# Optimization experiments

Hardware: AMD Instinct MI355X
Metric: run time of the kernel (lower is better)

## Reference

```python
import jax, jax.numpy as jnp
import numpy as np

HIDDEN = 256   # HIDDEN_NUM
INPUT = 4      # fixed input_size
B, T = 128, 512


def _lstm_dir(xs, wi, wh, bi, bh):
    """Single-direction LSTM scan. xs: [T,B,D]; wi: [4H,D]; wh: [4H,H]; bi,bh: [4H].
    PyTorch gate order: i, f, g, o. Returns hidden states [T,B,H]."""
    Tn, Bn, _ = xs.shape
    Hn = wh.shape[1]
    # precompute input contribution for all timesteps (tiny D -> one big GEMM)
    gx = jnp.einsum('tbd,gd->tbg', xs, wi) + bi + bh  # [T,B,4H]

    def step(carry, g):
        h, c = carry
        g = g + h @ wh.T
        i, f, gg, o = jnp.split(g, 4, axis=-1)
        c = jax.nn.sigmoid(f) * c + jax.nn.sigmoid(i) * jnp.tanh(gg)
        h = jax.nn.sigmoid(o) * jnp.tanh(c)
        return (h, c), h

    init = (jnp.zeros((Bn, Hn), xs.dtype), jnp.zeros((Bn, Hn), xs.dtype))
    _, hs = jax.lax.scan(step, init, gx)
    return hs


def _lstm_bidir(xs, w_ih, w_hh, b_ih, b_hh):
    """xs: [T,B,D]; weights stacked over direction: w_ih [2,4H,D] etc. -> [T,B,2H]."""
    fwd = _lstm_dir(xs, w_ih[0], w_hh[0], b_ih[0], b_hh[0])
    bwd = _lstm_dir(xs[::-1], w_ih[1], w_hh[1], b_ih[1], b_hh[1])[::-1]
    return jnp.concatenate([fwd, bwd], axis=-1)


def setup_inputs() -> dict:
    key = jax.random.key(0)
    ks = jax.random.split(key, 12)
    k = 1.0 / np.sqrt(HIDDEN)
    u = lambda kk, shape: jax.random.uniform(kk, shape, jnp.float32, -k, k)
    H4 = 4 * HIDDEN
    return {
        'x': jax.random.normal(ks[0], (B, T, INPUT), jnp.float32),
        # layer 0 (input size 4), stacked [fwd, bwd]
        'w_ih0': u(ks[1], (2, H4, INPUT)),
        'w_hh0': u(ks[2], (2, H4, HIDDEN)),
        'b_ih0': u(ks[3], (2, H4)),
        'b_hh0': u(ks[4], (2, H4)),
        # layer 1 (input size 2H from bidirectional layer 0)
        'w_ih1': u(ks[5], (2, H4, 2 * HIDDEN)),
        'w_hh1': u(ks[6], (2, H4, HIDDEN)),
        'b_ih1': u(ks[7], (2, H4)),
        'b_hh1': u(ks[8], (2, H4)),
        # final linear: HIDDEN*2 -> 2
        'fc_w': u(ks[9], (2, 2 * HIDDEN)),
        'fc_b': u(ks[10], (2,)),
    }


def reference(x, w_ih0, w_hh0, b_ih0, b_hh0, w_ih1, w_hh1, b_ih1, b_hh1, fc_w, fc_b):
    xs = jnp.transpose(x, (1, 0, 2))                 # [T,B,4] (seq-major like torch)
    h0 = _lstm_bidir(xs, w_ih0, w_hh0, b_ih0, b_hh0)  # [T,B,2H]
    h1 = _lstm_bidir(h0, w_ih1, w_hh1, b_ih1, b_hh1)  # [T,B,2H]
    pooled = jnp.mean(h1, axis=0)                     # [B,2H]
    return pooled @ fc_w.T + fc_b                     # [B,2]
```

## Files before the change

### kernel.cpp

```cpp
#include <hip/hip_runtime.h>
#include <hip/hip_bf16.h>


typedef __bf16 bf16;
typedef __bf16 bf16x4 __attribute__((ext_vector_type(4)));
typedef __bf16 bf16x8 __attribute__((ext_vector_type(8)));
typedef float  f32x4  __attribute__((ext_vector_type(4)));
typedef unsigned int u32;
typedef unsigned long long u64;
typedef u64 u64x2 __attribute__((ext_vector_type(2)));

#define T_SEQ 512
#define BATCH 128
#define HID   256

#define H0_BYTES   67239936ULL
#define H1_OFF     H0_BYTES
#define POOL_OFF   (H1_OFF + 262144ULL)
#define WIHB_OFF   (POOL_OFF + 262144ULL)
#define FL0_OFF    (WIHB_OFF + 2097152ULL)
#define FL1_OFF    (FL0_OFF + 16384ULL)

#define MFMA16(a, b, c) __builtin_amdgcn_mfma_f32_16x16x32_bf16((a), (b), (c), 0, 0, 0)
#define AL(p)     __hip_atomic_load((p), __ATOMIC_RELAXED, __HIP_MEMORY_SCOPE_AGENT)
#define AS(p, v)  __hip_atomic_store((p), (v), __ATOMIC_RELAXED, __HIP_MEMORY_SCOPE_AGENT)

__device__ __forceinline__ float fsig(float v) {
    return __builtin_amdgcn_rcpf(1.0f + __expf(-v));
}
__device__ __forceinline__ float ftanh(float v) {
    float a = fabsf(v);
    float e = __expf(-2.0f * a);
    float r = (1.0f - e) * __builtin_amdgcn_rcpf(1.0f + e);
    return v < 0.0f ? -r : r;
}

__global__ void k_init(unsigned int* ws_u, int* flags0, int* flags1) {
    const int t = blockIdx.x * 256 + threadIdx.x;
    ws_u[t] = 0u;
    ws_u[(size_t)513 * 16384 + t] = 0u;
    unsigned int* h1u = ws_u + (H1_OFF / 4);
    h1u[t] = 0u;
    h1u[32768 + t] = 0u;
    if (t < 4096) flags0[t] = 0;
    if (t < 4096) flags1[t] = 0;
}

__global__ void k_prep(const float* __restrict__ w, bf16* __restrict__ o) {
    const int i = (blockIdx.x * 256 + threadIdx.x) * 4;
    const f32x4 v = *(const f32x4*)(w + i);
    bf16x4 r;
    r[0] = (bf16)v[0]; r[1] = (bf16)v[1]; r[2] = (bf16)v[2]; r[3] = (bf16)v[3];
    *(bf16x4*)(o + i) = r;
}

__global__ __launch_bounds__(256, 1) void k_l0(
    const float* __restrict__ x, const float* __restrict__ wih,
    const float* __restrict__ whh, const float* __restrict__ bih,
    const float* __restrict__ bhh, bf16* __restrict__ h0,
    int* __restrict__ flags)
{
    __shared__ __align__(16) bf16 Hs[4][16][24];

    const int blk = blockIdx.x;
    const int dir = blk >> 5, bh = (blk >> 4) & 1, g = blk & 15;
    const int tid = threadIdx.x, wave = tid >> 6, lane = tid & 63;
    const int l15 = lane & 15, q = lane >> 4;
    const int j = g * 16 + l15;

    bf16x8 Bf[4][8];
#pragma unroll
    for (int tg = 0; tg < 4; ++tg) {
        const float* wr = whh + ((size_t)(dir * 1024 + tg * 256 + j)) * 256 + q * 8;
#pragma unroll
        for (int kt = 0; kt < 8; ++kt) {
            f32x4 aa = *(const f32x4*)(wr + kt * 32);
            f32x4 bb = *(const f32x4*)(wr + kt * 32 + 4);
            bf16x8 f;
            f[0] = (bf16)aa[0]; f[1] = (bf16)aa[1]; f[2] = (bf16)aa[2]; f[3] = (bf16)aa[3];
            f[4] = (bf16)bb[0]; f[5] = (bf16)bb[1]; f[6] = (bf16)bb[2]; f[7] = (bf16)bb[3];
            Bf[tg][kt] = f;
        }
    }
    float biasg[4], wx[4][4];
#pragma unroll
    for (int tg = 0; tg < 4; ++tg) {
        const int n = dir * 1024 + tg * 256 + j;
        biasg[tg] = bih[n] + bhh[n];
#pragma unroll
        for (int d2 = 0; d2 < 4; ++d2) wx[tg][d2] = wih[(size_t)n * 4 + d2];
    }

    float c4[4] = {0.f, 0.f, 0.f, 0.f};
    const int arow  = bh * 64 + wave * 16 + l15;
    const int mrow0 = bh * 64 + wave * 16 + q * 4;
    const int srow = lane >> 2, scg = (lane & 3) * 4;
    int* fgrp = flags + (dir * 2 + bh) * 1024;
    int budget = 100000000;

#pragma unroll 1
    for (int s = 1; s <= T_SEQ; ++s) {
        const int t_in = dir ? (T_SEQ - s) : (s - 1);

        f32x4 xv[4];
#pragma unroll
        for (int r = 0; r < 4; ++r)
            xv[r] = *(const f32x4*)(x + ((size_t)(mrow0 + r) * T_SEQ + t_in) * 4);
        f32x4 acc[4];
#pragma unroll
        for (int tg = 0; tg < 4; ++tg) {
#pragma unroll
            for (int r = 0; r < 4; ++r) {
                acc[tg][r] = biasg[tg] + xv[r][0] * wx[tg][0] + xv[r][1] * wx[tg][1]
                                       + xv[r][2] * wx[tg][2] + xv[r][3] * wx[tg][3];
            }
        }

        if (lane < 16) {
            const int need = s - 1;
            while (AL(fgrp + (lane * 4 + wave) * 16) < need) {
                if (--budget < 0) break;
            }
        }
        asm volatile("" ::: "memory");

        const u64* hsrc = (const u64*)(h0 + ((size_t)(dir * 513 + (s - 1)) * BATCH + arow) * HID)
                          + q * 2;
        u64 av[16];
#pragma unroll
        for (int kt = 0; kt < 8; ++kt) {
            av[2 * kt]     = AL(hsrc + kt * 8);
            av[2 * kt + 1] = AL(hsrc + kt * 8 + 1);
        }
#pragma unroll
        for (int kt = 0; kt < 8; ++kt) {
            u64x2 t2; t2[0] = av[2 * kt]; t2[1] = av[2 * kt + 1];
            const bf16x8 A = __builtin_bit_cast(bf16x8, t2);
            acc[0] = MFMA16(A, Bf[0][kt], acc[0]);
            acc[1] = MFMA16(A, Bf[1][kt], acc[1]);
            acc[2] = MFMA16(A, Bf[2][kt], acc[2]);
            acc[3] = MFMA16(A, Bf[3][kt], acc[3]);
        }

#pragma unroll
        for (int r = 0; r < 4; ++r) {
            const float iv = fsig(acc[0][r]);
            const float fv = fsig(acc[1][r]);
            const float gv = ftanh(acc[2][r]);
            const float ov = fsig(acc[3][r]);
            c4[r] = fv * c4[r] + iv * gv;
            const float hv = ov * ftanh(c4[r]);
            Hs[wave][q * 4 + r][l15] = (bf16)hv;
        }
        asm volatile("s_waitcnt lgkmcnt(0)" ::: "memory");
        {
            const u64 hv8 = *(const u64*)&Hs[wave][srow][scg];
            u64* dst = (u64*)(h0 + ((size_t)(dir * 513 + s) * BATCH
                              + bh * 64 + wave * 16 + srow) * HID + g * 16 + scg);
            AS(dst, hv8);
        }
        asm volatile("s_waitcnt vmcnt(0)" ::: "memory");
        if (lane == 0) AS(fgrp + (g * 4 + wave) * 16, s);
    }
}

__global__ __launch_bounds__(256, 1) void k_l1(
    const float* __restrict__ whh1, const float* __restrict__ bih1,
    const float* __restrict__ bhh1, const bf16* __restrict__ wihb,
    bf16* __restrict__ h0, bf16* __restrict__ h1,
    float* __restrict__ pooled, int* __restrict__ flags)
{
    __shared__ __align__(16) bf16 Hs[4][16][24];

    const int blk = blockIdx.x;
    const int dir = blk >> 5, bh = (blk >> 4) & 1, g = blk & 15;
    const int tid = threadIdx.x, wave = tid >> 6, lane = tid & 63;
    const int l15 = lane & 15, q = lane >> 4;
    const int j = g * 16 + l15;

    bf16x8 Bf[4][8];
#pragma unroll
    for (int tg = 0; tg < 4; ++tg) {
        const float* wr = whh1 + ((size_t)(dir * 1024 + tg * 256 + j)) * 256 + q * 8;
#pragma unroll
        for (int kt = 0; kt < 8; ++kt) {
            f32x4 aa = *(const f32x4*)(wr + kt * 32);
            f32x4 bb = *(const f32x4*)(wr + kt * 32 + 4);
            bf16x8 f;
            f[0] = (bf16)aa[0]; f[1] = (bf16)aa[1]; f[2] = (bf16)aa[2]; f[3] = (bf16)aa[3];
            f[4] = (bf16)bb[0]; f[5] = (bf16)bb[1]; f[6] = (bf16)bb[2]; f[7] = (bf16)bb[3];
            Bf[tg][kt] = f;
        }
    }
    float biasg[4];
#pragma unroll
    for (int tg = 0; tg < 4; ++tg) {
        const int n = dir * 1024 + tg * 256 + j;
        biasg[tg] = bih1[n] + bhh1[n];
    }

    float c4[4] = {0.f, 0.f, 0.f, 0.f};
    float pool[4] = {0.f, 0.f, 0.f, 0.f};
    const int arow = bh * 64 + wave * 16 + l15;
    const int srow = lane >> 2, scg = (lane & 3) * 4;
    const bf16* wb = wihb + ((size_t)(dir * 1024 + j)) * 512 + q * 8;
    int* fgrp = flags + (dir * 2 + bh) * 1024;
    int budget = 100000000;

#pragma unroll 1
    for (int s = 1; s <= T_SEQ; ++s) {
        const int slotf = dir ? (513 - s) : s;
        const int slotb = dir ? s : (513 - s);

        f32x4 acc[4];
#pragma unroll
        for (int tg = 0; tg < 4; ++tg) {
            acc[tg][0] = biasg[tg]; acc[tg][1] = biasg[tg];
            acc[tg][2] = biasg[tg]; acc[tg][3] = biasg[tg];
        }
        const bf16* af = h0 + ((size_t)slotf * BATCH + arow) * HID + q * 8;
        const bf16* ab = h0 + ((size_t)(513 + slotb) * BATCH + arow) * HID + q * 8;
#pragma unroll
        for (int kt = 0; kt < 8; ++kt) {
            const bf16x8 A = *(const bf16x8*)(af + kt * 32);
            acc[0] = MFMA16(A, *(const bf16x8*)(wb + 0 * 131072 + kt * 32), acc[0]);
            acc[1] = MFMA16(A, *(const bf16x8*)(wb + 1 * 131072 + kt * 32), acc[1]);
            acc[2] = MFMA16(A, *(const bf16x8*)(wb + 2 * 131072 + kt * 32), acc[2]);
            acc[3] = MFMA16(A, *(const bf16x8*)(wb + 3 * 131072 + kt * 32), acc[3]);
        }
#pragma unroll
        for (int kt = 0; kt < 8; ++kt) {
            const bf16x8 A = *(const bf16x8*)(ab + kt * 32);
            acc[0] = MFMA16(A, *(const bf16x8*)(wb + 256 + 0 * 131072 + kt * 32), acc[0]);
            acc[1] = MFMA16(A, *(const bf16x8*)(wb + 256 + 1 * 131072 + kt * 32), acc[1]);
            acc[2] = MFMA16(A, *(const bf16x8*)(wb + 256 + 2 * 131072 + kt * 32), acc[2]);
            acc[3] = MFMA16(A, *(const bf16x8*)(wb + 256 + 3 * 131072 + kt * 32), acc[3]);
        }

        if (lane < 16) {
            const int need = s - 1;
            while (AL(fgrp + (lane * 4 + wave) * 16) < need) {
                if (--budget < 0) break;
            }
        }
        asm volatile("" ::: "memory");

        const u64* hp = (const u64*)(h1 + ((size_t)(dir * 2 + ((s - 1) & 1)) * BATCH + arow) * HID)
                        + q * 2;
        u64 av[16];
#pragma unroll
        for (int kt = 0; kt < 8; ++kt) {
            av[2 * kt]     = AL(hp + kt * 8);
            av[2 * kt + 1] = AL(hp + kt * 8 + 1);
        }
#pragma unroll
        for (int kt = 0; kt < 8; ++kt) {
            u64x2 t2; t2[0] = av[2 * kt]; t2[1] = av[2 * kt + 1];
            const bf16x8 A = __builtin_bit_cast(bf16x8, t2);
            acc[0] = MFMA16(A, Bf[0][kt], acc[0]);
            acc[1] = MFMA16(A, Bf[1][kt], acc[1]);
            acc[2] = MFMA16(A, Bf[2][kt], acc[2]);
            acc[3] = MFMA16(A, Bf[3][kt], acc[3]);
        }

#pragma unroll
        for (int r = 0; r < 4; ++r) {
            const float iv = fsig(acc[0][r]);
            const float fv = fsig(acc[1][r]);
            const float gv = ftanh(acc[2][r]);
            const float ov = fsig(acc[3][r]);
            c4[r] = fv * c4[r] + iv * gv;
            const float hv = ov * ftanh(c4[r]);
            pool[r] += hv;
            Hs[wave][q * 4 + r][l15] = (bf16)hv;
        }
        asm volatile("s_waitcnt lgkmcnt(0)" ::: "memory");
        {
            const u64 hv8 = *(const u64*)&Hs[wave][srow][scg];
            u64* dst = (u64*)(h1 + ((size_t)(dir * 2 + (s & 1)) * BATCH
                              + bh * 64 + wave * 16 + srow) * HID + g * 16 + scg);
            AS(dst, hv8);
        }
        asm volatile("s_waitcnt vmcnt(0)" ::: "memory");
        if (lane == 0) AS(fgrp + (g * 4 + wave) * 16, s);
    }
#pragma unroll
    for (int r = 0; r < 4; ++r) {
        pooled[((size_t)dir * BATCH + bh * 64 + wave * 16 + q * 4 + r) * HID + j] =
            pool[r] * (1.0f / 512.0f);
    }
}

__global__ void k_fc(const float* __restrict__ pooled, const float* __restrict__ fcw,
                     const float* __restrict__ fcb, float* __restrict__ out)
{
    const int b = blockIdx.x;
    const int lane = threadIdx.x;
    float s0 = 0.f, s1 = 0.f;
#pragma unroll
    for (int jj = 0; jj < 8; ++jj) {
        const int jx = lane + jj * 64;
        const float p = (jx < 256) ? pooled[(size_t)b * 256 + jx]
                                   : pooled[32768 + (size_t)b * 256 + (jx - 256)];
        s0 += p * fcw[jx];
        s1 += p * fcw[512 + jx];
    }
#pragma unroll
    for (int off = 32; off > 0; off >>= 1) {
        s0 += __shfl_down(s0, off);
        s1 += __shfl_down(s1, off);
    }
    if (lane == 0) {
        out[b * 2 + 0] = s0 + fcb[0];
        out[b * 2 + 1] = s1 + fcb[1];
    }
}

extern "C" void kernel_launch(void* const* d_in, const int* in_sizes, int n_in,
                              void* d_out, int out_size, void* d_ws, size_t ws_size,
                              hipStream_t stream)
{
    const float* x    = (const float*)d_in[0];
    const float* wih0 = (const float*)d_in[1];
    const float* whh0 = (const float*)d_in[2];
    const float* bih0 = (const float*)d_in[3];
    const float* bhh0 = (const float*)d_in[4];
    const float* wih1 = (const float*)d_in[5];
    const float* whh1 = (const float*)d_in[6];
    const float* bih1 = (const float*)d_in[7];
    const float* bhh1 = (const float*)d_in[8];
    const float* fcw  = (const float*)d_in[9];
    const float* fcb  = (const float*)d_in[10];
    float* out = (float*)d_out;

    char* ws = (char*)d_ws;
    bf16* h0      = (bf16*)ws;
    bf16* h1      = (bf16*)(ws + H1_OFF);
    float* pooled = (float*)(ws + POOL_OFF);
    bf16* wihb    = (bf16*)(ws + WIHB_OFF);
    int* flags0   = (int*)(ws + FL0_OFF);
    int* flags1   = (int*)(ws + FL1_OFF);

    k_init<<<dim3(64), dim3(256), 0, stream>>>((unsigned int*)ws, flags0, flags1);
    k_prep<<<dim3(1024), dim3(256), 0, stream>>>(wih1, wihb);
    k_l0<<<dim3(64), dim3(256), 0, stream>>>(x, wih0, whh0, bih0, bhh0, h0, flags0);
    k_l1<<<dim3(64), dim3(256), 0, stream>>>(whh1, bih1, bhh1, wihb, h0, h1, pooled, flags1);
    k_fc<<<dim3(128), dim3(64), 0, stream>>>(pooled, fcw, fcb, out);
}
```

Measured before the change: 5.752 ms.

## Stage layer-1 input weights in LDS and coarsen layer-0 sync flags per block

Layer 1 now converts its slice of the input-projection weights to bf16 once per block and keeps it in shared memory. This removes the separate prep kernel and the per-step global reloads of those weights. Layer 0 now publishes one flag per block after a __syncthreads, instead of one flag per wave, so consumers poll 16 flags rather than 64. The change adds 64KB of LDS use and two block barriers per step in layer 0. The spin budget is also reduced.

```diff
diff --git a/kernel.cpp b/kernel.cpp
--- a/kernel.cpp
+++ b/kernel.cpp
@@ -3,7 +3,6 @@
 
 
 typedef __bf16 bf16;
-typedef __bf16 bf16x4 __attribute__((ext_vector_type(4)));
 typedef __bf16 bf16x8 __attribute__((ext_vector_type(8)));
 typedef float  f32x4  __attribute__((ext_vector_type(4)));
 typedef unsigned int u32;
@@ -17,9 +16,8 @@
 #define H0_BYTES   67239936ULL
 #define H1_OFF     H0_BYTES
 #define POOL_OFF   (H1_OFF + 262144ULL)
-#define WIHB_OFF   (POOL_OFF + 262144ULL)
-#define FL0_OFF    (WIHB_OFF + 2097152ULL)
-#define FL1_OFF    (FL0_OFF + 16384ULL)
+#define FL0_OFF    (POOL_OFF + 262144ULL)
+#define FL1_OFF    (FL0_OFF + 4096ULL)
 
 #define MFMA16(a, b, c) __builtin_amdgcn_mfma_f32_16x16x32_bf16((a), (b), (c), 0, 0, 0)
 #define AL(p)     __hip_atomic_load((p), __ATOMIC_RELAXED, __HIP_MEMORY_SCOPE_AGENT)
@@ -33,6 +31,18 @@
     float e = __expf(-2.0f * a);
     float r = (1.0f - e) * __builtin_amdgcn_rcpf(1.0f + e);
     return v < 0.0f ? -r : r;
+}
+__device__ __forceinline__ bf16x8 cvt8(const float* p) {
+    f32x4 aa = *(const f32x4*)p;
+    f32x4 bb = *(const f32x4*)(p + 4);
+    bf16x8 f;
+    f[0] = (bf16)aa[0]; f[1] = (bf16)aa[1]; f[2] = (bf16)aa[2]; f[3] = (bf16)aa[3];
+    f[4] = (bf16)bb[0]; f[5] = (bf16)bb[1]; f[6] = (bf16)bb[2]; f[7] = (bf16)bb[3];
+    return f;
+}
+__device__ __forceinline__ bf16x8 mk_a(u64 lo, u64 hi) {
+    u64x2 t; t[0] = lo; t[1] = hi;
+    return __builtin_bit_cast(bf16x8, t);
 }
 
 __global__ void k_init(unsigned int* ws_u, int* flags0, int* flags1) {
@@ -42,16 +52,8 @@
     unsigned int* h1u = ws_u + (H1_OFF / 4);
     h1u[t] = 0u;
     h1u[32768 + t] = 0u;
-    if (t < 4096) flags0[t] = 0;
+    if (t < 1024) flags0[t] = 0;
     if (t < 4096) flags1[t] = 0;
-}
-
-__global__ void k_prep(const float* __restrict__ w, bf16* __restrict__ o) {
-    const int i = (blockIdx.x * 256 + threadIdx.x) * 4;
-    const f32x4 v = *(const f32x4*)(w + i);
-    bf16x4 r;
-    r[0] = (bf16)v[0]; r[1] = (bf16)v[1]; r[2] = (bf16)v[2]; r[3] = (bf16)v[3];
-    *(bf16x4*)(o + i) = r;
 }
 
 __global__ __launch_bounds__(256, 1) void k_l0(
@@ -60,7 +62,7 @@
     const float* __restrict__ bhh, bf16* __restrict__ h0,
     int* __restrict__ flags)
 {
-    __shared__ __align__(16) bf16 Hs[4][16][24];
+    __shared__ __align__(16) bf16 Hs[64][20];
 
     const int blk = blockIdx.x;
     const int dir = blk >> 5, bh = (blk >> 4) & 1, g = blk & 15;
@@ -73,14 +75,7 @@
     for (int tg = 0; tg < 4; ++tg) {
         const float* wr = whh + ((size_t)(dir * 1024 + tg * 256 + j)) * 256 + q * 8;
 #pragma unroll
-        for (int kt = 0; kt < 8; ++kt) {
-            f32x4 aa = *(const f32x4*)(wr + kt * 32);
-            f32x4 bb = *(const f32x4*)(wr + kt * 32 + 4);
-            bf16x8 f;
-            f[0] = (bf16)aa[0]; f[1] = (bf16)aa[1]; f[2] = (bf16)aa[2]; f[3] = (bf16)aa[3];
-            f[4] = (bf16)bb[0]; f[5] = (bf16)bb[1]; f[6] = (bf16)bb[2]; f[7] = (bf16)bb[3];
-            Bf[tg][kt] = f;
-        }
+        for (int kt = 0; kt < 8; ++kt) Bf[tg][kt] = cvt8(wr + kt * 32);
     }
     float biasg[4], wx[4][4];
 #pragma unroll
@@ -93,10 +88,11 @@
 
     float c4[4] = {0.f, 0.f, 0.f, 0.f};
     const int arow  = bh * 64 + wave * 16 + l15;
-    const int mrow0 = bh * 64 + wave * 16 + q * 4;
-    const int srow = lane >> 2, scg = (lane & 3) * 4;
-    int* fgrp = flags + (dir * 2 + bh) * 1024;
-    int budget = 100000000;
+    const int lrow0 = wave * 16 + q * 4;
+    const int mrow0 = bh * 64 + lrow0;
+    const int srow = tid >> 2, scg = (tid & 3) * 4;
+    int* fgrp = flags + (dir * 2 + bh) * 256;
+    int budget = 30000000;
 
 #pragma unroll 1
     for (int s = 1; s <= T_SEQ; ++s) {
@@ -118,7 +114,7 @@
 
         if (lane < 16) {
             const int need = s - 1;
-            while (AL(fgrp + (lane * 4 + wave) * 16) < need) {
+            while (AL(fgrp + lane * 16) < need) {
                 if (--budget < 0) break;
             }
         }
@@ -134,8 +130,7 @@
         }
 #pragma unroll
         for (int kt = 0; kt < 8; ++kt) {
-            u64x2 t2; t2[0] = av[2 * kt]; t2[1] = av[2 * kt + 1];
-            const bf16x8 A = __builtin_bit_cast(bf16x8, t2);
+            const bf16x8 A = mk_a(av[2 * kt], av[2 * kt + 1]);
             acc[0] = MFMA16(A, Bf[0][kt], acc[0]);
             acc[1] = MFMA16(A, Bf[1][kt], acc[1]);
             acc[2] = MFMA16(A, Bf[2][kt], acc[2]);
@@ -150,26 +145,27 @@
             const float ov = fsig(acc[3][r]);
             c4[r] = fv * c4[r] + iv * gv;
             const float hv = ov * ftanh(c4[r]);
-            Hs[wave][q * 4 + r][l15] = (bf16)hv;
-        }
-        asm volatile("s_waitcnt lgkmcnt(0)" ::: "memory");
+            Hs[lrow0 + r][l15] = (bf16)hv;
+        }
+        __syncthreads();
         {
-            const u64 hv8 = *(const u64*)&Hs[wave][srow][scg];
-            u64* dst = (u64*)(h0 + ((size_t)(dir * 513 + s) * BATCH
-                              + bh * 64 + wave * 16 + srow) * HID + g * 16 + scg);
+            const u64 hv8 = *(const u64*)&Hs[srow][scg];
+            u64* dst = (u64*)(h0 + ((size_t)(dir * 513 + s) * BATCH + bh * 64 + srow) * HID
+                              + g * 16 + scg);
             AS(dst, hv8);
         }
-        asm volatile("s_waitcnt vmcnt(0)" ::: "memory");
-        if (lane == 0) AS(fgrp + (g * 4 + wave) * 16, s);
+        __syncthreads();
+        if (tid == 0) AS(fgrp + g * 16, s);
     }
 }
 
 __global__ __launch_bounds__(256, 1) void k_l1(
-    const float* __restrict__ whh1, const float* __restrict__ bih1,
-    const float* __restrict__ bhh1, const bf16* __restrict__ wihb,
+    const float* __restrict__ wih1, const float* __restrict__ whh1,
+    const float* __restrict__ bih1, const float* __restrict__ bhh1,
     bf16* __restrict__ h0, bf16* __restrict__ h1,
     float* __restrict__ pooled, int* __restrict__ flags)
 {
+    __shared__ __align__(16) bf16 WL[4][16][512];
     __shared__ __align__(16) bf16 Hs[4][16][24];
 
     const int blk = blockIdx.x;
@@ -178,19 +174,19 @@
     const int l15 = lane & 15, q = lane >> 4;
     const int j = g * 16 + l15;
 
+#pragma unroll
+    for (int c = 0; c < 16; ++c) {
+        const int tg = wave, kt2 = c;
+        const int n = dir * 1024 + tg * 256 + g * 16 + l15;
+        const float* src = wih1 + (size_t)n * 512 + kt2 * 32 + q * 8;
+        *(bf16x8*)&WL[tg][kt2][lane * 8] = cvt8(src);
+    }
     bf16x8 Bf[4][8];
 #pragma unroll
     for (int tg = 0; tg < 4; ++tg) {
         const float* wr = whh1 + ((size_t)(dir * 1024 + tg * 256 + j)) * 256 + q * 8;
 #pragma unroll
-        for (int kt = 0; kt < 8; ++kt) {
-            f32x4 aa = *(const f32x4*)(wr + kt * 32);
-            f32x4 bb = *(const f32x4*)(wr + kt * 32 + 4);
-            bf16x8 f;
-            f[0] = (bf16)aa[0]; f[1] = (bf16)aa[1]; f[2] = (bf16)aa[2]; f[3] = (bf16)aa[3];
-            f[4] = (bf16)bb[0]; f[5] = (bf16)bb[1]; f[6] = (bf16)bb[2]; f[7] = (bf16)bb[3];
-            Bf[tg][kt] = f;
-        }
+        for (int kt = 0; kt < 8; ++kt) Bf[tg][kt] = cvt8(wr + kt * 32);
     }
     float biasg[4];
 #pragma unroll
@@ -198,14 +194,15 @@
         const int n = dir * 1024 + tg * 256 + j;
         biasg[tg] = bih1[n] + bhh1[n];
     }
+    __syncthreads();
 
     float c4[4] = {0.f, 0.f, 0.f, 0.f};
     float pool[4] = {0.f, 0.f, 0.f, 0.f};
-    const int arow = bh * 64 + wave * 16 + l15;
+    const int arow  = bh * 64 + wave * 16 + l15;
+    const int mrow0 = bh * 64 + wave * 16 + q * 4;
     const int srow = lane >> 2, scg = (lane & 3) * 4;
-    const bf16* wb = wihb + ((size_t)(dir * 1024 + j)) * 512 + q * 8;
     int* fgrp = flags + (dir * 2 + bh) * 1024;
-    int budget = 100000000;
+    int budget = 30000000;
 
 #pragma unroll 1
     for (int s = 1; s <= T_SEQ; ++s) {
@@ -223,18 +220,18 @@
 #pragma unroll
         for (int kt = 0; kt < 8; ++kt) {
             const bf16x8 A = *(const bf16x8*)(af + kt * 32);
-            acc[0] = MFMA16(A, *(const bf16x8*)(wb + 0 * 131072 + kt * 32), acc[0]);
-            acc[1] = MFMA16(A, *(const bf16x8*)(wb + 1 * 131072 + kt * 32), acc[1]);
-            acc[2] = MFMA16(A, *(const bf16x8*)(wb + 2 * 131072 + kt * 32), acc[2]);
-            acc[3] = MFMA16(A, *(const bf16x8*)(wb + 3 * 131072 + kt * 32), acc[3]);
+            acc[0] = MFMA16(A, *(const bf16x8*)&WL[0][kt][lane * 8], acc[0]);
+            acc[1] = MFMA16(A, *(const bf16x8*)&WL[1][kt][lane * 8], acc[1]);
+            acc[2] = MFMA16(A, *(const bf16x8*)&WL[2][kt][lane * 8], acc[2]);
+            acc[3] = MFMA16(A, *(const bf16x8*)&WL[3][kt][lane * 8], acc[3]);
         }
 #pragma unroll
         for (int kt = 0; kt < 8; ++kt) {
             const bf16x8 A = *(const bf16x8*)(ab + kt * 32);
-            acc[0] = MFMA16(A, *(const bf16x8*)(wb + 256 + 0 * 131072 + kt * 32), acc[0]);
-            acc[1] = MFMA16(A, *(const bf16x8*)(wb + 256 + 1 * 131072 + kt * 32), acc[1]);
-            acc[2] = MFMA16(A, *(const bf16x8*)(wb + 256 + 2 * 131072 + kt * 32), acc[2]);
-            acc[3] = MFMA16(A, *(const bf16x8*)(wb + 256 + 3 * 131072 + kt * 32), acc[3]);
+            acc[0] = MFMA16(A, *(const bf16x8*)&WL[0][8 + kt][lane * 8], acc[0]);
+            acc[1] = MFMA16(A, *(const bf16x8*)&WL[1][8 + kt][lane * 8], acc[1]);
+            acc[2] = MFMA16(A, *(const bf16x8*)&WL[2][8 + kt][lane * 8], acc[2]);
+            acc[3] = MFMA16(A, *(const bf16x8*)&WL[3][8 + kt][lane * 8], acc[3]);
         }
 
         if (lane < 16) {
@@ -255,8 +252,7 @@
         }
 #pragma unroll
         for (int kt = 0; kt < 8; ++kt) {
-            u64x2 t2; t2[0] = av[2 * kt]; t2[1] = av[2 * kt + 1];
-            const bf16x8 A = __builtin_bit_cast(bf16x8, t2);
+            const bf16x8 A = mk_a(av[2 * kt], av[2 * kt + 1]);
             acc[0] = MFMA16(A, Bf[0][kt], acc[0]);
             acc[1] = MFMA16(A, Bf[1][kt], acc[1]);
             acc[2] = MFMA16(A, Bf[2][kt], acc[2]);
@@ -286,7 +282,7 @@
     }
 #pragma unroll
     for (int r = 0; r < 4; ++r) {
-        pooled[((size_t)dir * BATCH + bh * 64 + wave * 16 + q * 4 + r) * HID + j] =
+        pooled[((size_t)dir * BATCH + mrow0 + r) * HID + j] =
             pool[r] * (1.0f / 512.0f);
     }
 }
@@ -337,13 +333,11 @@
     bf16* h0      = (bf16*)ws;
     bf16* h1      = (bf16*)(ws + H1_OFF);
     float* pooled = (float*)(ws + POOL_OFF);
-    bf16* wihb    = (bf16*)(ws + WIHB_OFF);
     int* flags0   = (int*)(ws + FL0_OFF);
     int* flags1   = (int*)(ws + FL1_OFF);
 
     k_init<<<dim3(64), dim3(256), 0, stream>>>((unsigned int*)ws, flags0, flags1);
-    k_prep<<<dim3(1024), dim3(256), 0, stream>>>(wih1, wihb);
     k_l0<<<dim3(64), dim3(256), 0, stream>>>(x, wih0, whh0, bih0, bhh0, h0, flags0);
-    k_l1<<<dim3(64), dim3(256), 0, stream>>>(whh1, bih1, bhh1, wihb, h0, h1, pooled, flags1);
+    k_l1<<<dim3(64), dim3(256), 0, stream>>>(wih1, whh1, bih1, bhh1, h0, h1, pooled, flags1);
     k_fc<<<dim3(128), dim3(64), 0, stream>>>(pooled, fcw, fcb, out);
 }
```

New measurement: 4.879 ms. 15.2% less time.
